# Performance work log

Measured on AMD Instinct MI355X. Metric: run time of the kernel, lower is better.

## Reference

```python
import jax, jax.numpy as jnp
import numpy as np

D = 1024  # input_dim


def setup_inputs() -> dict:
    key = jax.random.key(0)
    ks = jax.random.split(key, 7)
    s = 1.0 / np.sqrt(D)
    return {
        "x": jax.random.normal(ks[0], (4, 2048, D), dtype=jnp.float32),
        "wq": jax.random.normal(ks[1], (D, D), dtype=jnp.float32) * s,
        "bq": jax.random.normal(ks[2], (D,), dtype=jnp.float32) * s,
        "wk": jax.random.normal(ks[3], (D, D), dtype=jnp.float32) * s,
        "bk": jax.random.normal(ks[4], (D,), dtype=jnp.float32) * s,
        "wv": jax.random.normal(ks[5], (D, D), dtype=jnp.float32) * s,
        "bv": jax.random.normal(ks[6], (D,), dtype=jnp.float32) * s,
    }


def reference(x, wq, bq, wk, bk, wv, bv):
    # torch Linear: y = x @ W^T + b
    q = jnp.einsum('btd,ed->bte', x, wq) + bq  # (B,T,D)
    k = jnp.einsum('btd,ed->bte', x, wk) + bk
    v = jnp.einsum('btd,ed->bte', x, wv) + bv
    scale = 1.0 / jnp.sqrt(jnp.asarray(D, dtype=x.dtype))
    scores = jnp.einsum('btd,bsd->bts', q, k) * scale  # (B,T,T)
    attn = jax.nn.softmax(scores, axis=-1)
    return jnp.einsum('bts,bsd->btd', attn, v)
```

## Files before the change

kernel.cpp:

```cpp
#include <hip/hip_runtime.h>
#include <stdint.h>

#define BB 4
#define TT 2048
#define DD 1024

typedef unsigned short u16;
typedef unsigned int u32;
typedef u16 u16x4 __attribute__((ext_vector_type(4)));
typedef u16 u16x8 __attribute__((ext_vector_type(8)));
typedef float f32x4 __attribute__((ext_vector_type(4)));
typedef short s16x8 __attribute__((ext_vector_type(8)));

__device__ __forceinline__ u16 f2bf(float f) {
  u32 u = __float_as_uint(f);
  return (u16)((u + 0x7fffu + ((u >> 16) & 1u)) >> 16);
}
__device__ __forceinline__ float bf2f(u16 h) {
  return __uint_as_float((u32)h << 16);
}

__device__ __forceinline__ void gload_lds16(const void* g, void* l) {
  __builtin_amdgcn_global_load_lds(
      (const __attribute__((address_space(1))) u32*)g,
      (__attribute__((address_space(3))) u32*)l, 16, 0, 0);
}

__device__ __forceinline__ void swz(int BMv, int BNv, int& tileM, int& tileN) {
  const int gN = gridDim.x, gM = gridDim.y;
  const int L = blockIdx.y * gN + blockIdx.x;
  const int xcd = L & 7, j = L >> 3;
  const int Mq = gM >> 2, Nq = gN >> 1;
  tileM = (((xcd >> 1) * Mq) + j / Nq) * BMv;
  tileN = (((xcd & 1) * Nq) + j % Nq) * BNv;
}

__global__ __launch_bounds__(256) void prep_kernel(
    const float* __restrict__ x, const float* __restrict__ wq,
    const float* __restrict__ wk, const float* __restrict__ wv,
    const float* __restrict__ bq, const float* __restrict__ bk,
    const float* __restrict__ bv, u16* __restrict__ xbf,
    u16* __restrict__ wcat, float* __restrict__ bcat) {
  const int NX = BB * TT * DD / 8;
  const int NW = DD * DD / 8;
  int i = blockIdx.x * 256 + threadIdx.x;
  if (i < NX) {
    const f32x4* p = (const f32x4*)x;
    f32x4 a = p[2 * (size_t)i];
    f32x4 b = p[2 * (size_t)i + 1];
    u16x8 o;
    o[0] = f2bf(a[0]); o[1] = f2bf(a[1]); o[2] = f2bf(a[2]); o[3] = f2bf(a[3]);
    o[4] = f2bf(b[0]); o[5] = f2bf(b[1]); o[6] = f2bf(b[2]); o[7] = f2bf(b[3]);
    *(u16x8*)(xbf + 8 * (size_t)i) = o;
  } else if (i < NX + 3 * NW) {
    const int k = i - NX;
    const float* src = k < NW ? wq : (k < 2 * NW ? wk : wv);
    const int ii = k < NW ? k : (k < 2 * NW ? k - NW : k - 2 * NW);
    const f32x4* p = (const f32x4*)src;
    f32x4 a = p[2 * (size_t)ii];
    f32x4 b = p[2 * (size_t)ii + 1];
    u16x8 o;
    o[0] = f2bf(a[0]); o[1] = f2bf(a[1]); o[2] = f2bf(a[2]); o[3] = f2bf(a[3]);
    o[4] = f2bf(b[0]); o[5] = f2bf(b[1]); o[6] = f2bf(b[2]); o[7] = f2bf(b[3]);
    *(u16x8*)(wcat + 8 * (size_t)k) = o;
  } else {
    const int k = i - NX - 3 * NW;
    if (k < 3 * DD) {
      float v = k < DD ? bq[k] : (k < 2 * DD ? bk[k - DD] : bv[k - 2 * DD]);
      bcat[k] = v;
    }
  }
}

__device__ __forceinline__ void kloop_bt(
    const u16* __restrict__ A, const u16* __restrict__ B, int lda, int ldb,
    int K, int tileM, int tileN, u16* sA, u16* sB, f32x4 acc[4][4]) {
  const int tid = threadIdx.x;
  const int lane = tid & 63;
  const int wave = tid >> 6;
  const int quad = lane >> 4;
  const int l15 = lane & 15;
  const int wm = (wave >> 1) << 6;
  const int wn = (wave & 1) << 6;

  const u16 *gA[4], *gB[4];
  u16 *lA[4], *lB[4];
#pragma unroll
  for (int j = 0; j < 4; ++j) {
    const int ch = wave * 256 + j * 64 + lane;
    const int r = ch >> 3;
    const int cg = ((ch & 7) ^ (r & 7)) * 8;
    gA[j] = A + (size_t)(tileM + r) * lda + cg;
    gB[j] = B + (size_t)(tileN + r) * ldb + cg;
    lA[j] = sA + wave * 2048 + j * 512;
    lB[j] = sB + wave * 2048 + j * 512;
  }

  const int x0 = (quad ^ (l15 & 7)) * 8;
  int aOff[4], bOff[4];
#pragma unroll
  for (int i = 0; i < 4; ++i) {
    aOff[i] = (wm + i * 16 + l15) * 64 + x0;
    bOff[i] = (wn + i * 16 + l15) * 64 + x0;
  }

  for (int it = 0; it < K; it += 64) {
#pragma unroll
    for (int j = 0; j < 4; ++j) gload_lds16(gA[j], lA[j]);
#pragma unroll
    for (int j = 0; j < 4; ++j) gload_lds16(gB[j], lB[j]);
#pragma unroll
    for (int j = 0; j < 4; ++j) { gA[j] += 64; gB[j] += 64; }
    __syncthreads();

    s16x8 af[4], bf[4];
#pragma unroll
    for (int i = 0; i < 4; ++i) af[i] = *(const s16x8*)(sA + aOff[i]);
#pragma unroll
    for (int i = 0; i < 4; ++i) bf[i] = *(const s16x8*)(sB + bOff[i]);
#pragma unroll
    for (int mi = 0; mi < 4; ++mi)
#pragma unroll
      for (int ni = 0; ni < 4; ++ni)
        acc[mi][ni] = __builtin_amdgcn_mfma_f32_16x16x32_bf16(
            af[mi], bf[ni], acc[mi][ni], 0, 0, 0);

#pragma unroll
    for (int i = 0; i < 4; ++i) af[i] = *(const s16x8*)(sA + (aOff[i] ^ 32));
#pragma unroll
    for (int i = 0; i < 4; ++i) bf[i] = *(const s16x8*)(sB + (bOff[i] ^ 32));
#pragma unroll
    for (int mi = 0; mi < 4; ++mi)
#pragma unroll
      for (int ni = 0; ni < 4; ++ni)
        acc[mi][ni] = __builtin_amdgcn_mfma_f32_16x16x32_bf16(
            af[mi], bf[ni], acc[mi][ni], 0, 0, 0);
    __syncthreads();
  }
}

__device__ __forceinline__ void kloop_dbc(
    const u16* __restrict__ A, const u16* __restrict__ B, int lda, int ldb,
    int K, int tileM, int tileN, u16* sm, f32x4 acc[4][4]) {
  const int tid = threadIdx.x;
  const int lane = tid & 63;
  const int wave = tid >> 6;
  const int quad = lane >> 4;
  const int l15 = lane & 15;
  const int wm = (wave >> 1) << 6;
  const int wn = (wave & 1) << 6;

  const u16 *gA[4], *gB[4];
  int lA[4], lB[4];
#pragma unroll
  for (int j = 0; j < 4; ++j) {
    const int ch = wave * 256 + j * 64 + lane;
    const int r = ch >> 3;
    const int cg = ((ch & 7) ^ (r & 7)) * 8;
    gA[j] = A + (size_t)(tileM + r) * lda + cg;
    gB[j] = B + (size_t)(tileN + r) * ldb + cg;
    lA[j] = wave * 2048 + j * 512;
    lB[j] = 8192 + wave * 2048 + j * 512;
  }

  const int x0 = (quad ^ (l15 & 7)) * 8;
  int aOff[4], bOff[4];
#pragma unroll
  for (int i = 0; i < 4; ++i) {
    aOff[i] = (wm + i * 16 + l15) * 64 + x0;
    bOff[i] = 8192 + (wn + i * 16 + l15) * 64 + x0;
  }

#pragma unroll
  for (int p = 0; p < 2; ++p) {
    u16* d = sm + p * 16384;
#pragma unroll
    for (int j = 0; j < 4; ++j) gload_lds16(gA[j], d + lA[j]);
#pragma unroll
    for (int j = 0; j < 4; ++j) gload_lds16(gB[j], d + lB[j]);
#pragma unroll
    for (int j = 0; j < 4; ++j) { gA[j] += 64; gB[j] += 64; }
  }

  const int NT = K >> 6;
  for (int t = 0; t < NT; ++t) {
    const u16* sb = sm + (t & 1) * 16384;
    u16* st = sm + (t & 1) * 16384;

    if (t + 1 < NT) {
      asm volatile("s_waitcnt vmcnt(8)" ::: "memory");
    } else {
      asm volatile("s_waitcnt vmcnt(0)" ::: "memory");
    }
    __builtin_amdgcn_s_barrier();
    __builtin_amdgcn_sched_barrier(0);

    s16x8 a0[4], b0[4], a1[4], b1[4];
#pragma unroll
    for (int i = 0; i < 4; ++i) a0[i] = *(const s16x8*)(sb + aOff[i]);
#pragma unroll
    for (int i = 0; i < 4; ++i) b0[i] = *(const s16x8*)(sb + bOff[i]);
#pragma unroll
    for (int i = 0; i < 4; ++i) a1[i] = *(const s16x8*)(sb + (aOff[i] ^ 32));
#pragma unroll
    for (int i = 0; i < 4; ++i) b1[i] = *(const s16x8*)(sb + (bOff[i] ^ 32));
    asm volatile("s_waitcnt lgkmcnt(0)" ::: "memory");
    __builtin_amdgcn_sched_barrier(0);
    __builtin_amdgcn_s_barrier();
    __builtin_amdgcn_sched_barrier(0);

    if (t + 2 < NT) {
#pragma unroll
      for (int j = 0; j < 4; ++j) gload_lds16(gA[j], st + lA[j]);
#pragma unroll
      for (int j = 0; j < 4; ++j) gload_lds16(gB[j], st + lB[j]);
#pragma unroll
      for (int j = 0; j < 4; ++j) { gA[j] += 64; gB[j] += 64; }
    }

    __builtin_amdgcn_s_setprio(1);
#pragma unroll
    for (int mi = 0; mi < 4; ++mi)
#pragma unroll
      for (int ni = 0; ni < 4; ++ni)
        acc[mi][ni] = __builtin_amdgcn_mfma_f32_16x16x32_bf16(
            a0[mi], b0[ni], acc[mi][ni], 0, 0, 0);
#pragma unroll
    for (int mi = 0; mi < 4; ++mi)
#pragma unroll
      for (int ni = 0; ni < 4; ++ni)
        acc[mi][ni] = __builtin_amdgcn_mfma_f32_16x16x32_bf16(
            a1[mi], b1[ni], acc[mi][ni], 0, 0, 0);
    __builtin_amdgcn_s_setprio(0);
  }
}

__global__ __launch_bounds__(256, 2) void gemm_qkv(
    const u16* __restrict__ A, const u16* __restrict__ B,
    u16* __restrict__ qk, u16* __restrict__ vt, const float* __restrict__ bias) {
  __shared__ u16 sA[128 * 64];
  __shared__ u16 sB[128 * 64];
  const int lane = threadIdx.x & 63;
  const int wave = threadIdx.x >> 6;
  const int quad = lane >> 4;
  const int l15 = lane & 15;
  const int wm = (wave >> 1) << 6;
  const int wn = (wave & 1) << 6;
  int tileM, tileN;
  swz(128, 128, tileM, tileN);

  f32x4 acc[4][4] = {};
  kloop_bt(A, B, DD, DD, DD, tileM, tileN, sA, sB, acc);

  const int rowB = tileM + wm + quad * 4;
  const int colB = tileN + wn + l15;
  if (tileN < 2048) {
    const float scale = (tileN < 1024) ? 0.03125f : 1.0f;
#pragma unroll
    for (int mi = 0; mi < 4; ++mi)
#pragma unroll
      for (int r = 0; r < 4; ++r) {
        u16* crow = qk + (size_t)(rowB + mi * 16 + r) * 2048 + colB;
#pragma unroll
        for (int ni = 0; ni < 4; ++ni)
          crow[ni * 16] = f2bf((acc[mi][ni][r] + bias[colB + ni * 16]) * scale);
      }
  } else {
    const int b = tileM >> 11;
    const int tBase = (rowB & 2047);
    u16* vb = vt + (size_t)b * DD * TT;
#pragma unroll
    for (int mi = 0; mi < 4; ++mi)
#pragma unroll
      for (int ni = 0; ni < 4; ++ni) {
        const int e = colB + ni * 16 - 2048;
        const float bs = bias[colB + ni * 16];
        u16x4 o;
#pragma unroll
        for (int r = 0; r < 4; ++r) o[r] = f2bf(acc[mi][ni][r] + bs);
        *(u16x4*)(vb + (size_t)e * TT + tBase + mi * 16) = o;
      }
  }
}

__global__ __launch_bounds__(256, 2) void gemm_s(
    const u16* __restrict__ qk, u16* __restrict__ sbuf,
    float* __restrict__ part) {
  __shared__ u16 sm[2 * 16384];
  const int lane = threadIdx.x & 63;
  const int wave = threadIdx.x >> 6;
  const int quad = lane >> 4;
  const int l15 = lane & 15;
  const int wm = (wave >> 1) << 6;
  const int wn = (wave & 1) << 6;
  int tileM, tileN;
  swz(128, 128, tileM, tileN);
  const int z = blockIdx.z;

  const u16* A = qk + (size_t)z * TT * 2048;
  const u16* B = qk + (size_t)z * TT * 2048 + 1024;

  f32x4 acc[4][4] = {};
  kloop_dbc(A, B, 2048, 2048, 1024, tileM, tileN, sm, acc);

  const int rowB = tileM + wm + quad * 4;
  const int colB = tileN + wn + l15;
  u16* C = sbuf + (size_t)z * TT * 2048;
  const int nIdx2 = (tileN + wn) >> 6;
  float* prow = part + ((size_t)z * 32 + nIdx2) * TT;
#pragma unroll
  for (int mi = 0; mi < 4; ++mi)
#pragma unroll
    for (int r = 0; r < 4; ++r) {
      const int row = rowB + mi * 16 + r;
      u16* crow = C + (size_t)row * 2048 + colB;
      float s = 0.f;
#pragma unroll
      for (int ni = 0; ni < 4; ++ni) {
        const u16 h = f2bf(__expf(acc[mi][ni][r]));
        crow[ni * 16] = h;
        s += bf2f(h);
      }
#pragma unroll
      for (int m = 1; m <= 8; m <<= 1) s += __shfl_xor(s, m, 64);
      if (l15 == 0) prow[row] = s;
    }
}

__global__ __launch_bounds__(256, 2) void gemm_pv(
    const u16* __restrict__ sbuf, const u16* __restrict__ vt,
    float* __restrict__ out, const float* __restrict__ part) {
  __shared__ u16 sm[2 * 16384];
  __shared__ float rowInv[128];
  const int tid = threadIdx.x;
  const int lane = tid & 63;
  const int wave = tid >> 6;
  const int quad = lane >> 4;
  const int l15 = lane & 15;
  const int wm = (wave >> 1) << 6;
  const int wn = (wave & 1) << 6;
  int tileM, tileN;
  swz(128, 128, tileM, tileN);
  const int z = blockIdx.z;

  if (tid < 128) {
    const float* pp = part + (size_t)z * 32 * TT + tileM + tid;
    float s = 0.f;
#pragma unroll
    for (int j = 0; j < 32; ++j) s += pp[j * TT];
    rowInv[tid] = 1.0f / s;
  }
  __syncthreads();

  const u16* A = sbuf + (size_t)z * TT * 2048;
  const u16* B = vt + (size_t)z * DD * TT;

  f32x4 acc[4][4] = {};
  kloop_dbc(A, B, 2048, TT, TT, tileM, tileN, sm, acc);

  const int rowB = tileM + wm + quad * 4;
  const int colB = tileN + wn + l15;
  float* C = out + (size_t)z * TT * DD;
#pragma unroll
  for (int mi = 0; mi < 4; ++mi)
#pragma unroll
    for (int r = 0; r < 4; ++r) {
      const int lrow = wm + quad * 4 + mi * 16 + r;
      const float inv = rowInv[lrow];
      float* crow = C + (size_t)(rowB + mi * 16 + r) * DD + colB;
#pragma unroll
      for (int ni = 0; ni < 4; ++ni) crow[ni * 16] = acc[mi][ni][r] * inv;
    }
}

extern "C" void kernel_launch(void* const* d_in, const int* in_sizes, int n_in,
                              void* d_out, int out_size, void* d_ws,
                              size_t ws_size, hipStream_t stream) {
  const float* x = (const float*)d_in[0];
  const float* wq = (const float*)d_in[1];
  const float* bq = (const float*)d_in[2];
  const float* wk = (const float*)d_in[3];
  const float* bk = (const float*)d_in[4];
  const float* wv = (const float*)d_in[5];
  const float* bv = (const float*)d_in[6];
  float* out = (float*)d_out;

  const size_t MB = 1024 * 1024;
  if (ws_size < 103 * MB) return;
  char* ws = (char*)d_ws;
  u16* xbf = (u16*)(ws);
  float* part = (float*)(ws);
  u16* wcat = (u16*)(ws + 16 * MB);
  float* bcat = (float*)(ws + 22 * MB);
  u16* qk = (u16*)(ws + 23 * MB);
  u16* vt = (u16*)(ws + 55 * MB);
  u16* sbuf = (u16*)(ws + 71 * MB);

  const dim3 blk256(256);

  prep_kernel<<<4096 + 1536 + 12, blk256, 0, stream>>>(
      x, wq, wk, wv, bq, bk, bv, xbf, wcat, bcat);

  gemm_qkv<<<dim3(3 * DD / 128, BB * TT / 128, 1), blk256, 0, stream>>>(
      xbf, wcat, qk, vt, bcat);

  gemm_s<<<dim3(TT / 128, TT / 128, BB), blk256, 0, stream>>>(qk, sbuf, part);

  gemm_pv<<<dim3(DD / 128, TT / 128, BB), blk256, 0, stream>>>(
      sbuf, vt, out, part);
}
```

Before: 231.1 us.

## Enlarge score GEMM tile to 256x256 with 8-wave phased LDS pipeline

The QK^T score kernel moves from 128x128 tiles with 4 waves to 256x256 tiles with 8 waves (512 threads). A new k-loop loads A and B halves in four phases, interleaving global-to-LDS prefetch into a double buffer with MFMA blocks and barriers. The aim is to raise arithmetic intensity and cut global traffic per FLOP for the score GEMM. In exchange it uses 128KB of LDS per block and more accumulator registers, which lowers occupancy, and the grid shrinks to 256 blocks.

```diff
diff --git a/kernel.cpp b/kernel.cpp
--- a/kernel.cpp
+++ b/kernel.cpp
@@ -235,6 +235,170 @@
   }
 }
 
+__device__ __forceinline__ void kloop_8ph(
+    const u16* __restrict__ A, const u16* __restrict__ B, int lda, int ldb,
+    int K, int tileM, int tileN, u16* sm, f32x4 (&acc)[8][4]) {
+  constexpr int AE = 16384;
+  constexpr int BUF = 32768;
+  const int tid = threadIdx.x;
+  const int lane = tid & 63;
+  const int wave = tid >> 6;
+  const int quad = lane >> 4;
+  const int l15 = lane & 15;
+  const int wm = (wave >> 2) << 7;
+  const int wn = (wave & 3) << 6;
+
+  const int rloc = tid >> 3;
+  const int cg = ((tid & 7) ^ (rloc & 7)) * 8;
+  const int ldst = tid * 8;
+
+  const u16* gA[4];
+  const u16* gB[4];
+#pragma unroll
+  for (int j = 0; j < 4; ++j) {
+    gA[j] = A + (size_t)(tileM + j * 64 + rloc) * lda + cg;
+    gB[j] = B + (size_t)(tileN + j * 64 + rloc) * ldb + cg;
+  }
+
+  const int x0 = (quad ^ (l15 & 7)) * 8;
+  int aOff[8], bOff[4];
+#pragma unroll
+  for (int i = 0; i < 8; ++i) aOff[i] = (wm + i * 16 + l15) * 64 + x0;
+#pragma unroll
+  for (int i = 0; i < 4; ++i) bOff[i] = AE + (wn + i * 16 + l15) * 64 + x0;
+
+#pragma unroll
+  for (int j = 0; j < 4; ++j) gload_lds16(gA[j], sm + j * 4096 + ldst);
+#pragma unroll
+  for (int j = 0; j < 4; ++j) gload_lds16(gB[j], sm + AE + j * 4096 + ldst);
+#pragma unroll
+  for (int j = 0; j < 4; ++j) { gA[j] += 64; gB[j] += 64; }
+#pragma unroll
+  for (int j = 0; j < 4; ++j)
+    gload_lds16(gB[j], sm + BUF + AE + j * 4096 + ldst);
+#pragma unroll
+  for (int j = 0; j < 4; ++j) gB[j] += 64;
+  asm volatile("s_waitcnt vmcnt(4)" ::: "memory");
+  __builtin_amdgcn_s_barrier();
+  __builtin_amdgcn_sched_barrier(0);
+
+  const int NT = K >> 6;
+  for (int t = 0; t < NT; ++t) {
+    const u16* sb = sm + (t & 1) * BUF;
+    u16* sbW = sm + (t & 1) * BUF;
+    u16* soW = sm + ((t + 1) & 1) * BUF;
+    const bool stA = (t + 1 < NT);
+    const bool stB = (t + 2 < NT);
+    s16x8 aL[4][2], aH[4][2], bL[2][2], bH[2][2];
+
+#pragma unroll
+    for (int i = 0; i < 4; ++i) {
+      aL[i][0] = *(const s16x8*)(sb + aOff[i]);
+      aL[i][1] = *(const s16x8*)(sb + (aOff[i] ^ 32));
+    }
+#pragma unroll
+    for (int j = 0; j < 2; ++j) {
+      bL[j][0] = *(const s16x8*)(sb + bOff[j]);
+      bL[j][1] = *(const s16x8*)(sb + (bOff[j] ^ 32));
+    }
+    if (stA) {
+      gload_lds16(gA[0], soW + 0 * 4096 + ldst);
+      gload_lds16(gA[1], soW + 1 * 4096 + ldst);
+    }
+    __builtin_amdgcn_s_barrier();
+    asm volatile("s_waitcnt lgkmcnt(0)" ::: "memory");
+    __builtin_amdgcn_sched_barrier(0);
+    __builtin_amdgcn_s_setprio(1);
+#pragma unroll
+    for (int mi = 0; mi < 4; ++mi)
+#pragma unroll
+      for (int ni = 0; ni < 2; ++ni)
+#pragma unroll
+        for (int ks = 0; ks < 2; ++ks)
+          acc[mi][ni] = __builtin_amdgcn_mfma_f32_16x16x32_bf16(
+              aL[mi][ks], bL[ni][ks], acc[mi][ni], 0, 0, 0);
+    __builtin_amdgcn_s_setprio(0);
+    __builtin_amdgcn_s_barrier();
+    __builtin_amdgcn_sched_barrier(0);
+
+#pragma unroll
+    for (int j = 0; j < 2; ++j) {
+      bH[j][0] = *(const s16x8*)(sb + bOff[2 + j]);
+      bH[j][1] = *(const s16x8*)(sb + (bOff[2 + j] ^ 32));
+    }
+    if (stA) {
+      gload_lds16(gA[2], soW + 2 * 4096 + ldst);
+      gload_lds16(gA[3], soW + 3 * 4096 + ldst);
+#pragma unroll
+      for (int j = 0; j < 4; ++j) gA[j] += 64;
+    }
+    __builtin_amdgcn_s_barrier();
+    asm volatile("s_waitcnt lgkmcnt(0)" ::: "memory");
+    __builtin_amdgcn_sched_barrier(0);
+    __builtin_amdgcn_s_setprio(1);
+#pragma unroll
+    for (int mi = 0; mi < 4; ++mi)
+#pragma unroll
+      for (int ni = 0; ni < 2; ++ni)
+#pragma unroll
+        for (int ks = 0; ks < 2; ++ks)
+          acc[mi][2 + ni] = __builtin_amdgcn_mfma_f32_16x16x32_bf16(
+              aL[mi][ks], bH[ni][ks], acc[mi][2 + ni], 0, 0, 0);
+    __builtin_amdgcn_s_setprio(0);
+    __builtin_amdgcn_s_barrier();
+    __builtin_amdgcn_sched_barrier(0);
+
+#pragma unroll
+    for (int i = 0; i < 4; ++i) {
+      aH[i][0] = *(const s16x8*)(sb + aOff[4 + i]);
+      aH[i][1] = *(const s16x8*)(sb + (aOff[4 + i] ^ 32));
+    }
+    if (stB) {
+      gload_lds16(gB[0], sbW + AE + 0 * 4096 + ldst);
+      gload_lds16(gB[1], sbW + AE + 1 * 4096 + ldst);
+    }
+    __builtin_amdgcn_s_barrier();
+    asm volatile("s_waitcnt lgkmcnt(0)" ::: "memory");
+    __builtin_amdgcn_sched_barrier(0);
+    __builtin_amdgcn_s_setprio(1);
+#pragma unroll
+    for (int mi = 0; mi < 4; ++mi)
+#pragma unroll
+      for (int ni = 0; ni < 2; ++ni)
+#pragma unroll
+        for (int ks = 0; ks < 2; ++ks)
+          acc[4 + mi][ni] = __builtin_amdgcn_mfma_f32_16x16x32_bf16(
+              aH[mi][ks], bL[ni][ks], acc[4 + mi][ni], 0, 0, 0);
+    __builtin_amdgcn_s_setprio(0);
+    __builtin_amdgcn_s_barrier();
+    __builtin_amdgcn_sched_barrier(0);
+
+    if (stB) {
+      gload_lds16(gB[2], sbW + AE + 2 * 4096 + ldst);
+      gload_lds16(gB[3], sbW + AE + 3 * 4096 + ldst);
+#pragma unroll
+      for (int j = 0; j < 4; ++j) gB[j] += 64;
+    }
+    __builtin_amdgcn_s_setprio(1);
+#pragma unroll
+    for (int mi = 0; mi < 4; ++mi)
+#pragma unroll
+      for (int ni = 0; ni < 2; ++ni)
+#pragma unroll
+        for (int ks = 0; ks < 2; ++ks)
+          acc[4 + mi][2 + ni] = __builtin_amdgcn_mfma_f32_16x16x32_bf16(
+              aH[mi][ks], bH[ni][ks], acc[4 + mi][2 + ni], 0, 0, 0);
+    __builtin_amdgcn_s_setprio(0);
+    if (stB) {
+      asm volatile("s_waitcnt vmcnt(4)" ::: "memory");
+    } else if (stA) {
+      asm volatile("s_waitcnt vmcnt(0)" ::: "memory");
+    }
+    __builtin_amdgcn_s_barrier();
+    __builtin_amdgcn_sched_barrier(0);
+  }
+}
+
 __global__ __launch_bounds__(256, 2) void gemm_qkv(
     const u16* __restrict__ A, const u16* __restrict__ B,
     u16* __restrict__ qk, u16* __restrict__ vt, const float* __restrict__ bias) {
@@ -283,25 +447,25 @@
   }
 }
 
-__global__ __launch_bounds__(256, 2) void gemm_s(
+__global__ __launch_bounds__(512, 2) void gemm_s(
     const u16* __restrict__ qk, u16* __restrict__ sbuf,
     float* __restrict__ part) {
-  __shared__ u16 sm[2 * 16384];
+  __shared__ u16 sm[2 * 32768];
   const int lane = threadIdx.x & 63;
   const int wave = threadIdx.x >> 6;
   const int quad = lane >> 4;
   const int l15 = lane & 15;
-  const int wm = (wave >> 1) << 6;
-  const int wn = (wave & 1) << 6;
+  const int wm = (wave >> 2) << 7;
+  const int wn = (wave & 3) << 6;
   int tileM, tileN;
-  swz(128, 128, tileM, tileN);
+  swz(256, 256, tileM, tileN);
   const int z = blockIdx.z;
 
   const u16* A = qk + (size_t)z * TT * 2048;
   const u16* B = qk + (size_t)z * TT * 2048 + 1024;
 
-  f32x4 acc[4][4] = {};
-  kloop_dbc(A, B, 2048, 2048, 1024, tileM, tileN, sm, acc);
+  f32x4 acc[8][4] = {};
+  kloop_8ph(A, B, 2048, 2048, 1024, tileM, tileN, sm, acc);
 
   const int rowB = tileM + wm + quad * 4;
   const int colB = tileN + wn + l15;
@@ -309,7 +473,7 @@
   const int nIdx2 = (tileN + wn) >> 6;
   float* prow = part + ((size_t)z * 32 + nIdx2) * TT;
 #pragma unroll
-  for (int mi = 0; mi < 4; ++mi)
+  for (int mi = 0; mi < 8; ++mi)
 #pragma unroll
     for (int r = 0; r < 4; ++r) {
       const int row = rowB + mi * 16 + r;
@@ -397,6 +561,7 @@
   u16* sbuf = (u16*)(ws + 71 * MB);
 
   const dim3 blk256(256);
+  const dim3 blk512(512);
 
   prep_kernel<<<4096 + 1536 + 12, blk256, 0, stream>>>(
       x, wq, wk, wv, bq, bk, bv, xbf, wcat, bcat);
@@ -404,7 +569,7 @@
   gemm_qkv<<<dim3(3 * DD / 128, BB * TT / 128, 1), blk256, 0, stream>>>(
       xbf, wcat, qk, vt, bcat);
 
-  gemm_s<<<dim3(TT / 128, TT / 128, BB), blk256, 0, stream>>>(qk, sbuf, part);
+  gemm_s<<<dim3(TT / 256, TT / 256, BB), blk512, 0, stream>>>(qk, sbuf, part);
 
   gemm_pv<<<dim3(DD / 128, TT / 128, BB), blk256, 0, stream>>>(
       sbuf, vt, out, part);
```

Result: no change. 233.1 us (+0.9%).

## Fuse fp32-to-bf16 conversion of x into QKV GEMM A-tile loads

Applied to the files above, without the earlier changes.

The prep kernel no longer converts x to bf16. The QKV GEMM now reads fp32 x directly from global memory, converts it to bf16 in registers and writes it to LDS, while the weights still use async global-to-LDS loads. This removes a full write and re-read of the 16MB bf16 copy of x. In exchange, each A tile is re-read as fp32 by all 24 N-tiles, doubling A traffic in the GEMM, and the loads become synchronous register round-trips instead of direct-to-LDS transfers.

```diff
diff --git a/kernel.cpp b/kernel.cpp
--- a/kernel.cpp
+++ b/kernel.cpp
@@ -36,35 +36,24 @@
 }
 
 __global__ __launch_bounds__(256) void prep_kernel(
-    const float* __restrict__ x, const float* __restrict__ wq,
-    const float* __restrict__ wk, const float* __restrict__ wv,
-    const float* __restrict__ bq, const float* __restrict__ bk,
-    const float* __restrict__ bv, u16* __restrict__ xbf,
+    const float* __restrict__ wq, const float* __restrict__ wk,
+    const float* __restrict__ wv, const float* __restrict__ bq,
+    const float* __restrict__ bk, const float* __restrict__ bv,
     u16* __restrict__ wcat, float* __restrict__ bcat) {
-  const int NX = BB * TT * DD / 8;
   const int NW = DD * DD / 8;
   int i = blockIdx.x * 256 + threadIdx.x;
-  if (i < NX) {
-    const f32x4* p = (const f32x4*)x;
-    f32x4 a = p[2 * (size_t)i];
-    f32x4 b = p[2 * (size_t)i + 1];
-    u16x8 o;
-    o[0] = f2bf(a[0]); o[1] = f2bf(a[1]); o[2] = f2bf(a[2]); o[3] = f2bf(a[3]);
-    o[4] = f2bf(b[0]); o[5] = f2bf(b[1]); o[6] = f2bf(b[2]); o[7] = f2bf(b[3]);
-    *(u16x8*)(xbf + 8 * (size_t)i) = o;
-  } else if (i < NX + 3 * NW) {
-    const int k = i - NX;
-    const float* src = k < NW ? wq : (k < 2 * NW ? wk : wv);
-    const int ii = k < NW ? k : (k < 2 * NW ? k - NW : k - 2 * NW);
+  if (i < 3 * NW) {
+    const float* src = i < NW ? wq : (i < 2 * NW ? wk : wv);
+    const int ii = i < NW ? i : (i < 2 * NW ? i - NW : i - 2 * NW);
     const f32x4* p = (const f32x4*)src;
     f32x4 a = p[2 * (size_t)ii];
     f32x4 b = p[2 * (size_t)ii + 1];
     u16x8 o;
     o[0] = f2bf(a[0]); o[1] = f2bf(a[1]); o[2] = f2bf(a[2]); o[3] = f2bf(a[3]);
     o[4] = f2bf(b[0]); o[5] = f2bf(b[1]); o[6] = f2bf(b[2]); o[7] = f2bf(b[3]);
-    *(u16x8*)(wcat + 8 * (size_t)k) = o;
+    *(u16x8*)(wcat + 8 * (size_t)i) = o;
   } else {
-    const int k = i - NX - 3 * NW;
+    const int k = i - 3 * NW;
     if (k < 3 * DD) {
       float v = k < DD ? bq[k] : (k < 2 * DD ? bk[k - DD] : bv[k - 2 * DD]);
       bcat[k] = v;
@@ -72,8 +61,8 @@
   }
 }
 
-__device__ __forceinline__ void kloop_bt(
-    const u16* __restrict__ A, const u16* __restrict__ B, int lda, int ldb,
+__device__ __forceinline__ void kloop_bt_xA(
+    const float* __restrict__ A, const u16* __restrict__ B, int lda, int ldb,
     int K, int tileM, int tileN, u16* sA, u16* sB, f32x4 acc[4][4]) {
   const int tid = threadIdx.x;
   const int lane = tid & 63;
@@ -83,8 +72,9 @@
   const int wm = (wave >> 1) << 6;
   const int wn = (wave & 1) << 6;
 
-  const u16 *gA[4], *gB[4];
-  u16 *lA[4], *lB[4];
+  const float* gA[4];
+  const u16* gB[4];
+  u16 *lAw[4], *lB[4];
 #pragma unroll
   for (int j = 0; j < 4; ++j) {
     const int ch = wave * 256 + j * 64 + lane;
@@ -92,7 +82,7 @@
     const int cg = ((ch & 7) ^ (r & 7)) * 8;
     gA[j] = A + (size_t)(tileM + r) * lda + cg;
     gB[j] = B + (size_t)(tileN + r) * ldb + cg;
-    lA[j] = sA + wave * 2048 + j * 512;
+    lAw[j] = sA + wave * 2048 + j * 512 + lane * 8;
     lB[j] = sB + wave * 2048 + j * 512;
   }
 
@@ -106,9 +96,18 @@
 
   for (int it = 0; it < K; it += 64) {
 #pragma unroll
-    for (int j = 0; j < 4; ++j) gload_lds16(gA[j], lA[j]);
-#pragma unroll
     for (int j = 0; j < 4; ++j) gload_lds16(gB[j], lB[j]);
+#pragma unroll
+    for (int j = 0; j < 4; ++j) {
+      const f32x4 u0 = *(const f32x4*)gA[j];
+      const f32x4 u1 = *(const f32x4*)(gA[j] + 4);
+      u16x8 o;
+      o[0] = f2bf(u0[0]); o[1] = f2bf(u0[1]);
+      o[2] = f2bf(u0[2]); o[3] = f2bf(u0[3]);
+      o[4] = f2bf(u1[0]); o[5] = f2bf(u1[1]);
+      o[6] = f2bf(u1[2]); o[7] = f2bf(u1[3]);
+      *(u16x8*)lAw[j] = o;
+    }
 #pragma unroll
     for (int j = 0; j < 4; ++j) { gA[j] += 64; gB[j] += 64; }
     __syncthreads();
@@ -236,7 +235,7 @@
 }
 
 __global__ __launch_bounds__(256, 2) void gemm_qkv(
-    const u16* __restrict__ A, const u16* __restrict__ B,
+    const float* __restrict__ A, const u16* __restrict__ B,
     u16* __restrict__ qk, u16* __restrict__ vt, const float* __restrict__ bias) {
   __shared__ u16 sA[128 * 64];
   __shared__ u16 sB[128 * 64];
@@ -250,7 +249,7 @@
   swz(128, 128, tileM, tileN);
 
   f32x4 acc[4][4] = {};
-  kloop_bt(A, B, DD, DD, DD, tileM, tileN, sA, sB, acc);
+  kloop_bt_xA(A, B, DD, DD, DD, tileM, tileN, sA, sB, acc);
 
   const int rowB = tileM + wm + quad * 4;
   const int colB = tileN + wn + l15;
@@ -388,7 +387,6 @@
   const size_t MB = 1024 * 1024;
   if (ws_size < 103 * MB) return;
   char* ws = (char*)d_ws;
-  u16* xbf = (u16*)(ws);
   float* part = (float*)(ws);
   u16* wcat = (u16*)(ws + 16 * MB);
   float* bcat = (float*)(ws + 22 * MB);
@@ -398,11 +396,11 @@
 
   const dim3 blk256(256);
 
-  prep_kernel<<<4096 + 1536 + 12, blk256, 0, stream>>>(
-      x, wq, wk, wv, bq, bk, bv, xbf, wcat, bcat);
+  prep_kernel<<<1536 + 12, blk256, 0, stream>>>(
+      wq, wk, wv, bq, bk, bv, wcat, bcat);
 
   gemm_qkv<<<dim3(3 * DD / 128, BB * TT / 128, 1), blk256, 0, stream>>>(
-      xbf, wcat, qk, vt, bcat);
+      x, wcat, qk, vt, bcat);
 
   gemm_s<<<dim3(TT / 128, TT / 128, BB), blk256, 0, stream>>>(qk, sbuf, part);
 
```

Result: slower. 259.9 us (+12.5%).
